# Kernel optimization log

Hardware: AMD Instinct MI355X
Metric: run time of the kernel (lower is better)

## Reference

```python
import jax, jax.numpy as jnp
import numpy as np

MIN_NORM = 1e-15
PROJ_EPS = 4e-3


def _artanh(x):
    x = jnp.clip(x, -1 + 1e-7, 1 - 1e-7)
    return 0.5 * (jnp.log1p(x) - jnp.log1p(-x))


def _norm(x):
    return jnp.clip(jnp.linalg.norm(x, axis=-1, keepdims=True), MIN_NORM)


def proj(x, c):
    norm = _norm(x)
    maxnorm = (1.0 - PROJ_EPS) / jnp.sqrt(c)
    return jnp.where(norm > maxnorm, x / norm * maxnorm, x)


def expmap0(u, c):
    sqrt_c = jnp.sqrt(c)
    u_norm = _norm(u)
    return jnp.tanh(sqrt_c * u_norm) * u / (sqrt_c * u_norm)


def logmap0(p, c):
    sqrt_c = jnp.sqrt(c)
    p_norm = _norm(p)
    return _artanh(sqrt_c * p_norm) * p / (sqrt_c * p_norm)


def mobius_add(x, y, c):
    x2 = jnp.sum(x * x, axis=-1, keepdims=True)
    y2 = jnp.sum(y * y, axis=-1, keepdims=True)
    xy = jnp.sum(x * y, axis=-1, keepdims=True)
    num = (1 + 2 * c * xy + c * y2) * x + (1 - c * x2) * y
    denom = 1 + 2 * c * xy + c * c * x2 * y2
    return num / jnp.clip(denom, MIN_NORM)


def mobius_matvec(m, x, c):
    sqrt_c = jnp.sqrt(c)
    x_norm = _norm(x)
    mx = x @ m.T
    mx_norm = _norm(mx)
    res = jnp.tanh(mx_norm / x_norm * _artanh(sqrt_c * x_norm)) * mx / (mx_norm * sqrt_c)
    zero_row = jnp.all(mx == 0, axis=-1, keepdims=True)
    return jnp.where(zero_row, jnp.zeros_like(res), res)


def setup_inputs() -> dict:
    key = jax.random.key(0)
    k1, k2, k3, k4, k5 = jax.random.split(key, 5)
    n, d, e = 50000, 128, 800000
    c = jnp.float32(1.0)
    x = 0.1 * jax.random.normal(k1, (n, d), dtype=jnp.float32)
    x = proj(x, c)  # points on the Poincare ball
    adj = jax.random.randint(k2, (2, e), 0, n, dtype=jnp.int64)
    w = jax.random.uniform(k3, (e,), dtype=jnp.float32)
    weight = jax.random.normal(k4, (d, d), dtype=jnp.float32) * (1.0 / np.sqrt(d))
    bias = jax.random.normal(k5, (d,), dtype=jnp.float32) * 0.01
    return {"x": x, "adj": adj, "w": w, "weight": weight, "bias": bias}


def reference(x, adj, w, weight, bias):
    c_in = jnp.float32(1.0)
    c_out = jnp.float32(1.0)
    n = x.shape[0]

    # HypLinear (dropout p=0 -> identity on weight)
    mv = mobius_matvec(weight, x, c_in)
    res = proj(mv, c_in)
    b = bias.reshape(1, -1)  # proj_tan0 is identity on the Poincare ball
    hyp_bias = proj(expmap0(b, c_in), c_in)
    h = proj(mobius_add(res, hyp_bias, c_in), c_in)

    # HypAgg: logmap0 -> weighted segment_sum over edges -> expmap0 -> proj
    s, r = adj[0], adj[1]
    ht = logmap0(h, c_in)
    x_s = ht[s] * w[:, None]  # [E, d]
    x_agg = jax.ops.segment_sum(x_s, r, num_segments=n)
    h = proj(expmap0(x_agg, c_in), c_in)

    # HypAct: act(logmap0) -> expmap0 -> proj
    xt = jax.nn.relu(logmap0(h, c_in))
    out = proj(expmap0(xt, c_out), c_out)
    return (out, adj)
```

## Files before the change

kernel.cpp:

```cpp
#include <hip/hip_runtime.h>
#include <math.h>

#define MAXN 0.996f
#define MINN 1e-15f
#define CAP  5120

typedef __bf16   bf16x8  __attribute__((ext_vector_type(8)));
typedef _Float16 halfx8  __attribute__((ext_vector_type(8)));
typedef _Float16 half2_t __attribute__((ext_vector_type(2)));
typedef float    floatx4 __attribute__((ext_vector_type(4)));

__device__ __forceinline__ float wsum(float v){
  v += __shfl_xor(v, 32);
  v += __shfl_xor(v, 16);
  v += __shfl_xor(v, 8);
  v += __shfl_xor(v, 4);
  v += __shfl_xor(v, 2);
  v += __shfl_xor(v, 1);
  return v;
}

__device__ __forceinline__ float artanh_(float v){
  v = fminf(fmaxf(v, -1.f + 1e-7f), 1.f - 1e-7f);
  return 0.5f * (log1pf(v) - log1pf(-v));
}

__device__ __forceinline__ int block_excl_scan(int v, int tid, int* wsums){
  int lane = tid & 63, wid = tid >> 6;
  int iv = v;
#pragma unroll
  for(int o = 1; o < 64; o <<= 1){
    int t = __shfl_up(iv, o);
    if(lane >= o) iv += t;
  }
  if(lane == 63) wsums[wid] = iv;
  __syncthreads();
  int wbase = 0;
  for(int k = 0; k < wid; k++) wbase += wsums[k];
  return wbase + iv - v;
}

__global__ __launch_bounds__(256)
void fusedA_kernel(const float* __restrict__ x, const float* __restrict__ W,
                   const float* __restrict__ bias, _Float16* __restrict__ ht, int n,
                   const int* __restrict__ adj, const float* __restrict__ w,
                   float* __restrict__ adj_out, int* __restrict__ bucketSize,
                   int2* __restrict__ part, int E, int nA)
{
  __shared__ __align__(16) char smem[43264];
  const int tid = threadIdx.x;

  if(blockIdx.x < nA){
    int* hist  = (int*)smem;
    int* wcur  = (int*)(smem + 4096);
    int* lbase = (int*)(smem + 8192);
    int* gbase = (int*)(smem + 9216);
    int* wsA   = (int*)(smem + 10240);
    int2* stag = (int2*)(smem + 10256);

    const int wv = tid >> 6;
#pragma unroll
    for(int k = 0; k < 4; k++) hist[k*256 + tid] = 0;
    __syncthreads();

    const int e0 = blockIdx.x * 4096;
    int p0r[16], p1r[16];
#pragma unroll
    for(int k = 0; k < 16; k++){
      int e = e0 + k*256 + tid;
      if(e < E){
        int s = adj[e];
        int r = adj[e + E];
        float we = w[e];
        adj_out[e]     = (float)s;
        adj_out[e + E] = (float)r;
        int b = r >> 8;
        p0r[k] = s | ((r & 255) << 16) | (b << 24);
        p1r[k] = __float_as_int(we);
        atomicAdd(&hist[wv*256 + b], 1);
      }
    }
    __syncthreads();
    int h0 = hist[0*256+tid], h1 = hist[1*256+tid], h2 = hist[2*256+tid], h3 = hist[3*256+tid];
    int cb = h0 + h1 + h2 + h3;
    int lb = block_excl_scan(cb, tid, wsA);
    lbase[tid]      = lb;
    wcur[0*256+tid] = lb;
    wcur[1*256+tid] = lb + h0;
    wcur[2*256+tid] = lb + h0 + h1;
    wcur[3*256+tid] = lb + h0 + h1 + h2;
    gbase[tid] = cb ? atomicAdd(&bucketSize[tid], cb) : 0;
    __syncthreads();
#pragma unroll
    for(int k = 0; k < 16; k++){
      int e = e0 + k*256 + tid;
      if(e < E){
        int b = ((unsigned)p0r[k]) >> 24;
        int pos = atomicAdd(&wcur[wv*256 + b], 1);
        stag[pos] = make_int2(p0r[k], p1r[k]);
      }
    }
    __syncthreads();
    int total = (e0 + 4096 <= E) ? 4096 : (E - e0);
    for(int i = tid; i < total; i += 256){
      int2 p = stag[i];
      int b = ((unsigned)p.x) >> 24;
      int loc = gbase[b] + (i - lbase[b]);
      if(loc < CAP) part[(size_t)b * CAP + loc] = p;
    }
    return;
  }

  __bf16* Wh   = (__bf16*)smem;
  float* hb_sh = (float*)(smem + 32768);
  float* y2_sh = (float*)(smem + 33280);

  for(int g = tid; g < 2048; g += 256){
    int nr = g >> 4, k16 = g & 15;
    const float* wp = W + nr * 128 + k16 * 8;
    float4 a = *(const float4*)wp;
    float4 b = *(const float4*)(wp + 4);
    bf16x8 h;
    h[0]=(__bf16)a.x; h[1]=(__bf16)a.y; h[2]=(__bf16)a.z; h[3]=(__bf16)a.w;
    h[4]=(__bf16)b.x; h[5]=(__bf16)b.y; h[6]=(__bf16)b.z; h[7]=(__bf16)b.w;
    *(bf16x8*)&Wh[nr * 128 + ((k16 ^ (nr & 15)) << 3)] = h;
  }
  if(tid < 64){
    int l = tid;
    float b0 = bias[l], b1 = bias[l + 64];
    float bn = fmaxf(sqrtf(wsum(b0*b0 + b1*b1)), MINN);
    float sb = tanhf(bn) / bn;
    float hb0 = sb*b0, hb1 = sb*b1;
    float hnn = fmaxf(sqrtf(wsum(hb0*hb0 + hb1*hb1)), MINN);
    if(hnn > MAXN){ float f = MAXN/hnn; hb0 *= f; hb1 *= f; }
    float y2 = wsum(hb0*hb0 + hb1*hb1);
    hb_sh[l] = hb0; hb_sh[l + 64] = hb1;
    if(l == 0) *y2_sh = y2;
  }
  __syncthreads();

  const int lane = tid & 63;
  const int wid  = tid >> 6;
  const int q    = lane >> 4;
  const int n15  = lane & 15;

  const int M0 = (blockIdx.x - nA) * 64 + wid * 16;
  if(M0 >= n) return;

  float hbv[8];
#pragma unroll
  for(int t = 0; t < 8; t++) hbv[t] = hb_sh[t*16 + n15];
  const float y2 = *y2_sh;

  floatx4 acc[8];
#pragma unroll
  for(int t = 0; t < 8; t++) acc[t] = (floatx4){0.f,0.f,0.f,0.f};

  float x2p = 0.f;
  int m = M0 + n15; if(m > n - 1) m = n - 1;
#pragma unroll
  for(int kk = 0; kk < 4; kk++){
    const float* xp = x + (size_t)m * 128 + kk * 32 + q * 8;
    float4 xa = *(const float4*)xp;
    float4 xb = *(const float4*)(xp + 4);
    x2p += xa.x*xa.x + xa.y*xa.y + xa.z*xa.z + xa.w*xa.w
         + xb.x*xb.x + xb.y*xb.y + xb.z*xb.z + xb.w*xb.w;
    bf16x8 a;
    a[0]=(__bf16)xa.x; a[1]=(__bf16)xa.y; a[2]=(__bf16)xa.z; a[3]=(__bf16)xa.w;
    a[4]=(__bf16)xb.x; a[5]=(__bf16)xb.y; a[6]=(__bf16)xb.z; a[7]=(__bf16)xb.w;
    int k16 = kk * 4 + q;
#pragma unroll
    for(int t = 0; t < 8; t++){
      bf16x8 b = *(bf16x8*)&Wh[(t*16 + n15) * 128 + ((k16 ^ n15) << 3)];
      acc[t] = __builtin_amdgcn_mfma_f32_16x16x32_bf16(a, b, acc[t], 0, 0, 0);
    }
  }
  x2p += __shfl_xor(x2p, 16);
  x2p += __shfl_xor(x2p, 32);

  float mp[4], dp[4];
#pragma unroll
  for(int i = 0; i < 4; i++){
    float mpi = 0.f, dpi = 0.f;
#pragma unroll
    for(int t = 0; t < 8; t++){ float v = acc[t][i]; mpi = fmaf(v, v, mpi); dpi = fmaf(v, hbv[t], dpi); }
    mpi += __shfl_xor(mpi, 1); mpi += __shfl_xor(mpi, 2); mpi += __shfl_xor(mpi, 4); mpi += __shfl_xor(mpi, 8);
    dpi += __shfl_xor(dpi, 1); dpi += __shfl_xor(dpi, 2); dpi += __shfl_xor(dpi, 4); dpi += __shfl_xor(dpi, 8);
    mp[i] = mpi; dp[i] = dpi;
  }

  const int li   = lane & 3;
  const int srcl = (((lane >> 2) << 4) | li) & 63;
  float selmp = li==0 ? mp[0] : li==1 ? mp[1] : li==2 ? mp[2] : mp[3];
  float seldp = li==0 ? dp[0] : li==1 ? dp[1] : li==2 ? dp[2] : dp[3];
  float tmp_mp = __shfl(selmp, srcl);
  float tmp_dp = __shfl(seldp, srcl);
  float mxn = fmaxf(sqrtf(tmp_mp), MINN);
  float xn  = fmaxf(sqrtf(x2p), MINN);
  float tt  = tanhf(mxn / xn * artanh_(xn));
  float s1  = tt / mxn;
  float rn  = fmaxf(tt, MINN);
  if(rn > MAXN) s1 *= MAXN / rn;
  float xy    = s1 * tmp_dp;
  float r2    = s1 * s1 * tmp_mp;
  float alpha = 1.f + 2.f*xy + y2;
  float beta  = 1.f - r2;
  float inv   = 1.f / fmaxf(1.f + 2.f*xy + r2*y2, MINN);
  float as1   = alpha * s1;

  float as1b[4], betab[4], invb[4];
#pragma unroll
  for(int i = 0; i < 4; i++){
    int sl = ((lane >> 4) << 2) | i;
    as1b[i]  = __shfl(as1, sl);
    betab[i] = __shfl(beta, sl);
    invb[i]  = __shfl(inv, sl);
  }

  float uv[4][8];
  float u2[4];
#pragma unroll
  for(int i = 0; i < 4; i++){
    float u2i = 0.f;
#pragma unroll
    for(int t = 0; t < 8; t++){
      float u = (as1b[i] * acc[t][i] + betab[i] * hbv[t]) * invb[i];
      uv[i][t] = u;
      u2i = fmaf(u, u, u2i);
    }
    u2i += __shfl_xor(u2i, 1); u2i += __shfl_xor(u2i, 2); u2i += __shfl_xor(u2i, 4); u2i += __shfl_xor(u2i, 8);
    u2[i] = u2i;
  }

  float selu = li==0 ? u2[0] : li==1 ? u2[1] : li==2 ? u2[2] : u2[3];
  float tu   = __shfl(selu, srcl);
  float un = fmaxf(sqrtf(tu), MINN);
  float sc = 1.f, hn = un;
  if(un > MAXN){ sc = MAXN/un; hn = MAXN; }
  float lt = artanh_(hn) / hn * sc;

#pragma unroll
  for(int i = 0; i < 4; i++){
    int grow = M0 + q * 4 + i;
    float lti = __shfl(lt, ((lane >> 4) << 2) | i);
    if(grow < n){
      halfx8 f;
#pragma unroll
      for(int t = 0; t < 8; t++) f[t] = (_Float16)(lti * uv[i][t]);
      *(halfx8*)(ht + (size_t)grow * 128 + n15 * 8) = f;
    }
  }
}

__global__ __launch_bounds__(256)
void passB_kernel(const int* __restrict__ bucketSize, const int2* __restrict__ part,
                  unsigned* __restrict__ epk, int* __restrict__ offs, int n)
{
  __shared__ int sizes[256];
  __shared__ int hist[256];
  __shared__ int cursor[256];
  __shared__ int wsA[4];
  __shared__ int2 stag[CAP];

  const int tid = threadIdx.x;
  const int b   = blockIdx.x;
  sizes[tid] = bucketSize[tid];
  hist[tid]  = 0;
  __syncthreads();
  int sb = block_excl_scan(sizes[tid], tid, wsA);
  __shared__ int base_sh;
  if(tid == b) base_sh = sb;
  __syncthreads();
  const int base_b = base_sh;
  int size = sizes[b]; if(size > CAP) size = CAP;

  const int2* src = part + (size_t)b * CAP;
  for(int i = tid; i < size; i += 256){
    int2 p = src[i];
    stag[i] = p;
    atomicAdd(&hist[(((unsigned)p.x) >> 16) & 255], 1);
  }
  __syncthreads();
  int rb = block_excl_scan(hist[tid], tid, wsA);
  int grow = b * 256 + tid;
  if(grow <= n) offs[grow] = base_b + rb;
  cursor[tid] = rb;
  __syncthreads();
  for(int i = tid; i < size; i += 256){
    int2 p = stag[i];
    int rlo = (((unsigned)p.x) >> 16) & 255;
    int pos = atomicAdd(&cursor[rlo], 1);
    unsigned wh = (unsigned)__builtin_bit_cast(unsigned short,
                    (_Float16)__builtin_bit_cast(float, p.y));
    epk[base_b + pos] = (unsigned)(p.x & 0xFFFF) | (wh << 16);
  }
}

__global__ __launch_bounds__(256)
void agg_act_kernel(const int* __restrict__ offs, const unsigned* __restrict__ epk,
                    const _Float16* __restrict__ ht, float* __restrict__ out, int n)
{
  __shared__ float tr[4][128];
  int wid = threadIdx.x >> 6;
  int row = blockIdx.x * 4 + wid;
  if(row >= n) return;
  int lane = threadIdx.x & 63;
  int g = lane >> 4, i = lane & 15;
  int beg = offs[row];
  int m   = offs[row + 1] - beg;
  const unsigned* ep = epk + beg;
  const char* htb = (const char*)ht;
  const int ioff = i << 4;

  half2_t acc2[4];
#pragma unroll
  for(int k = 0; k < 4; k++) acc2[k] = (half2_t){(_Float16)0.f, (_Float16)0.f};

#define EDGE(pk) { \
    int s_ = (int)((pk) & 0xFFFFu); \
    half2_t w2_ = __builtin_bit_cast(half2_t, __builtin_amdgcn_perm(pk, pk, 0x03020302u)); \
    int4 q_ = *(const int4*)(htb + ((s_ << 8) | ioff)); \
    acc2[0] = __builtin_bit_cast(half2_t, q_.x) * w2_ + acc2[0]; \
    acc2[1] = __builtin_bit_cast(half2_t, q_.y) * w2_ + acc2[1]; \
    acc2[2] = __builtin_bit_cast(half2_t, q_.z) * w2_ + acc2[2]; \
    acc2[3] = __builtin_bit_cast(half2_t, q_.w) * w2_ + acc2[3]; \
  }

  int iters = (m + 3) >> 2;
  int it = 0;
  for(; it + 1 < iters; it += 2){
    int t0 = it*4 + g;
    int t1 = t0 + 4;
    unsigned pk0 = ep[t0];
    int tc1 = (t1 < m) ? t1 : (m - 1);
    unsigned pk1 = ep[tc1];
    if(t1 >= m) pk1 &= 0xFFFFu;
    EDGE(pk0);
    EDGE(pk1);
  }
  if(it < iters){
    int t0 = it*4 + g;
    int tc0 = (t0 < m) ? t0 : (m - 1);
    unsigned pk0 = ep[tc0];
    if(t0 >= m) pk0 &= 0xFFFFu;
    EDGE(pk0);
  }
#undef EDGE

  float acc[8];
#pragma unroll
  for(int k = 0; k < 4; k++){
    acc[2*k]   = (float)acc2[k][0];
    acc[2*k+1] = (float)acc2[k][1];
  }
#pragma unroll
  for(int k = 0; k < 8; k++){
    acc[k] += __shfl_xor(acc[k], 16);
    acc[k] += __shfl_xor(acc[k], 32);
  }

  float u2p = 0.f;
#pragma unroll
  for(int k = 0; k < 8; k++) u2p = fmaf(acc[k], acc[k], u2p);
  u2p += __shfl_xor(u2p, 1); u2p += __shfl_xor(u2p, 2);
  u2p += __shfl_xor(u2p, 4); u2p += __shfl_xor(u2p, 8);
  float un = fmaxf(sqrtf(u2p), MINN);
  float te = tanhf(un);
  float se = te / un;
  float gn = fmaxf(te, MINN);
  float hn = gn;
  if(gn > MAXN){ se *= MAXN/gn; hn = MAXN; }
  float la = artanh_(hn) / hn * se;
  float l[8];
  float r2p = 0.f;
#pragma unroll
  for(int k = 0; k < 8; k++){ l[k] = fmaxf(la*acc[k], 0.f); r2p = fmaf(l[k], l[k], r2p); }
  r2p += __shfl_xor(r2p, 1); r2p += __shfl_xor(r2p, 2);
  r2p += __shfl_xor(r2p, 4); r2p += __shfl_xor(r2p, 8);
  float rn = fmaxf(sqrtf(r2p), MINN);
  float t2 = tanhf(rn);
  float s2 = t2 / rn;
  float on = fmaxf(t2, MINN);
  if(on > MAXN) s2 *= MAXN/on;

  if(g == 0){
#pragma unroll
    for(int k = 0; k < 8; k++) tr[wid][k*16 + i] = s2 * l[k];
  }
  float2 o = *(float2*)&tr[wid][lane * 2];
  *(float2*)(out + (size_t)row * 128 + lane * 2) = o;
}

extern "C" void kernel_launch(void* const* d_in, const int* in_sizes, int n_in,
                              void* d_out, int out_size, void* d_ws, size_t ws_size,
                              hipStream_t stream)
{
  const float* x    = (const float*)d_in[0];
  const int*   adj  = (const int*)  d_in[1];
  const float* w    = (const float*)d_in[2];
  const float* W    = (const float*)d_in[3];
  const float* bias = (const float*)d_in[4];
  const int n = in_sizes[0] / 128;
  const int E = in_sizes[2];

  float* out     = (float*)d_out;
  float* adj_out = out + (size_t)n * 128;

  char* ws = (char*)d_ws;
  _Float16* ht   = (_Float16*)ws;  ws += (size_t)n * 128 * sizeof(_Float16);
  int2*  part    = (int2*)ws;      ws += (size_t)256 * CAP * sizeof(int2);
  unsigned* epk  = (unsigned*)ws;  ws += (size_t)E * sizeof(unsigned);
  int*   offs    = (int*)ws;       ws += (size_t)(n + 1) * sizeof(int);
  int*   bucketSize = (int*)ws;

  const int nA = (E + 4095) / 4096;
  const int nS = (n + 63) / 64;

  hipMemsetAsync(bucketSize, 0, 256 * sizeof(int), stream);
  fusedA_kernel<<<nA + nS, 256, 0, stream>>>(x, W, bias, ht, n,
                                             adj, w, adj_out, bucketSize, part, E, nA);
  passB_kernel<<<(n + 255) / 256, 256, 0, stream>>>(bucketSize, part, epk, offs, n);
  agg_act_kernel<<<(n + 3) / 4, 256, 0, stream>>>(offs, epk, ht, out, n);
}
```

Baseline: 160.7 us.

## Assign one row per 16-lane group in aggregation kernel instead of per wavefront

```diff
diff --git a/kernel.cpp b/kernel.cpp
--- a/kernel.cpp
+++ b/kernel.cpp
@@ -300,15 +300,12 @@
 void agg_act_kernel(const int* __restrict__ offs, const unsigned* __restrict__ epk,
                     const _Float16* __restrict__ ht, float* __restrict__ out, int n)
 {
-  __shared__ float tr[4][128];
-  int wid = threadIdx.x >> 6;
-  int row = blockIdx.x * 4 + wid;
-  if(row >= n) return;
-  int lane = threadIdx.x & 63;
-  int g = lane >> 4, i = lane & 15;
-  int beg = offs[row];
-  int m   = offs[row + 1] - beg;
-  const unsigned* ep = epk + beg;
+  __shared__ float tr[4][4][132];
+  const int tid  = threadIdx.x;
+  const int wid  = tid >> 6;
+  const int lane = tid & 63;
+  const int g = lane >> 4, i = lane & 15;
+  const int row = blockIdx.x * 16 + wid * 4 + g;
   const char* htb = (const char*)ht;
   const int ioff = i << 4;
 
@@ -326,24 +323,18 @@
     acc2[3] = __builtin_bit_cast(half2_t, q_.w) * w2_ + acc2[3]; \
   }
 
-  int iters = (m + 3) >> 2;
-  int it = 0;
-  for(; it + 1 < iters; it += 2){
-    int t0 = it*4 + g;
-    int t1 = t0 + 4;
-    unsigned pk0 = ep[t0];
-    int tc1 = (t1 < m) ? t1 : (m - 1);
-    unsigned pk1 = ep[tc1];
-    if(t1 >= m) pk1 &= 0xFFFFu;
-    EDGE(pk0);
-    EDGE(pk1);
-  }
-  if(it < iters){
-    int t0 = it*4 + g;
-    int tc0 = (t0 < m) ? t0 : (m - 1);
-    unsigned pk0 = ep[tc0];
-    if(t0 >= m) pk0 &= 0xFFFFu;
-    EDGE(pk0);
+  if(row < n){
+    int beg = offs[row];
+    int m   = offs[row + 1] - beg;
+    const unsigned* ep = epk + beg;
+    int t = 0;
+    for(; t + 1 < m; t += 2){
+      unsigned pk0 = ep[t];
+      unsigned pk1 = ep[t + 1];
+      EDGE(pk0);
+      EDGE(pk1);
+    }
+    if(t < m) EDGE(ep[t]);
   }
 #undef EDGE
 
@@ -353,12 +344,6 @@
     acc[2*k]   = (float)acc2[k][0];
     acc[2*k+1] = (float)acc2[k][1];
   }
-#pragma unroll
-  for(int k = 0; k < 8; k++){
-    acc[k] += __shfl_xor(acc[k], 16);
-    acc[k] += __shfl_xor(acc[k], 32);
-  }
-
   float u2p = 0.f;
 #pragma unroll
   for(int k = 0; k < 8; k++) u2p = fmaf(acc[k], acc[k], u2p);
@@ -383,12 +368,15 @@
   float on = fmaxf(t2, MINN);
   if(on > MAXN) s2 *= MAXN/on;
 
-  if(g == 0){
-#pragma unroll
-    for(int k = 0; k < 8; k++) tr[wid][k*16 + i] = s2 * l[k];
-  }
-  float2 o = *(float2*)&tr[wid][lane * 2];
-  *(float2*)(out + (size_t)row * 128 + lane * 2) = o;
+  if(row < n){
+#pragma unroll
+    for(int k = 0; k < 8; k++) tr[wid][g][k*16 + i] = s2 * l[k];
+    float4 o0 = *(float4*)&tr[wid][g][i*8];
+    float4 o1 = *(float4*)&tr[wid][g][i*8 + 4];
+    float* orow = out + (size_t)row * 128 + i*8;
+    *(float4*)orow       = o0;
+    *(float4*)(orow + 4) = o1;
+  }
 }
 
 extern "C" void kernel_launch(void* const* d_in, const int* in_sizes, int n_in,
@@ -420,5 +408,5 @@
   fusedA_kernel<<<nA + nS, 256, 0, stream>>>(x, W, bias, ht, n,
                                              adj, w, adj_out, bucketSize, part, E, nA);
   passB_kernel<<<(n + 255) / 256, 256, 0, stream>>>(bucketSize, part, epk, offs, n);
-  agg_act_kernel<<<(n + 3) / 4, 256, 0, stream>>>(offs, epk, ht, out, n);
-}
+  agg_act_kernel<<<(n + 15) / 16, 256, 0, stream>>>(offs, epk, ht, out, n);
+}
```

Result: faster. 153.8 us (-4.3%).
